# Optimization experiments

Measured on AMD Instinct MI355X. Metric: run time of the kernel, lower is better.

## Reference

```python
import jax, jax.numpy as jnp
import numpy as np

# ---- forest structure (static) ----
B = 32                      # number of trees in the batch
DEPTH = 12                  # topological levels per tree
LEVELS = [2 ** d for d in range(DEPTH)]           # nodes per level (root=level 0)
STARTS = np.concatenate([[0], np.cumsum(LEVELS)[:-1]]).astype(int)
NPG = int(sum(LEVELS))      # 4095 nodes per graph, node 0 = root
N = B * NPG                 # 131040 total nodes
VOCAB = 20000               # dataset.PAD_TOKEN_VALUE + 1
PAD = VOCAB - 1             # padding_idx
E = 256                     # embedding_dim (x_size)
H = 256                     # lstm_output_dim (h_size)
C = 104                     # num_classes (extra_non_linear=None)


def setup_inputs() -> dict:
    key = jax.random.key(0)
    ks = jax.random.split(key, 8)
    # random parent in the previous level for every non-root node (irregular fan-in)
    rng = np.random.RandomState(0)
    par = np.full(N, -1, dtype=np.int64)
    for g in range(B):
        off = g * NPG
        for d in range(1, DEPTH):
            nd = LEVELS[d]
            par[off + STARTS[d]: off + STARTS[d] + nd] = (
                off + STARTS[d - 1] + rng.randint(0, LEVELS[d - 1], size=nd))
    s = 0.05
    return {
        'x': jax.random.randint(ks[0], (N,), 0, VOCAB),
        'par': jnp.asarray(par),
        'emb': jax.random.normal(ks[1], (VOCAB, E), jnp.float32) * s,
        'W_iou': jax.random.normal(ks[2], (3 * H, E), jnp.float32) * s,
        'U_iou': jax.random.normal(ks[3], (3 * H, H), jnp.float32) * s,
        'b_iou': jnp.zeros((1, 3 * H), jnp.float32),
        'U_f_w': jax.random.normal(ks[4], (H, H), jnp.float32) * s,
        'U_f_b': jnp.zeros((H,), jnp.float32),
        'lin_w': jax.random.normal(ks[5], (C, H), jnp.float32) * s,
        'lin_b': jnp.zeros((C,), jnp.float32),
    }


def _forward(x, par, emb, W_iou, U_iou, b_iou, U_f_w, U_f_b, lin_w, lin_b):
    emb = emb.at[PAD].set(0.0)                 # padding_idx row is zero
    x_vec = emb[x]                             # [N, E]
    iou = x_vec @ W_iou.T                      # [N, 3H], W_iou has no bias
    h = jnp.zeros((N, H), x_vec.dtype)
    c = jnp.zeros((N, H), x_vec.dtype)
    offs = jnp.arange(B) * NPG
    # topological propagation: leaves (deepest level) -> root, per generation
    for d in range(DEPTH - 1, -1, -1):
        nd = LEVELS[d]
        nids = (offs[:, None] + STARTS[d] + jnp.arange(nd)).reshape(-1)  # [B*nd]
        iou_n = iou[nids]
        if d < DEPTH - 1:
            nc = LEVELS[d + 1]
            cids = (offs[:, None] + STARTS[d + 1] + jnp.arange(nc)).reshape(-1)
            h_ch = h[cids]                     # mailbox gather of child states
            c_ch = c[cids]
            p = par[cids]                      # global parent id per child
            seg = (p // NPG) * nd + (p % NPG - STARTS[d])  # parent slot in this level
            f = jax.nn.sigmoid(h_ch @ U_f_w.T + U_f_b)     # per-child forget gate
            h_tild = jax.ops.segment_sum(h_ch, seg, num_segments=B * nd)
            c_agg = jax.ops.segment_sum(f * c_ch, seg, num_segments=B * nd)
            iou_n = iou_n + h_tild @ U_iou.T
            c_n = c_agg
        else:
            c_n = jnp.zeros((B * nd, H), x_vec.dtype)
        iou_n = iou_n + b_iou
        i, o, u = jnp.split(iou_n, 3, axis=1)
        c_new = jax.nn.sigmoid(i) * jnp.tanh(u) + c_n
        h_new = jax.nn.sigmoid(o) * jnp.tanh(c_new)
        h = h.at[nids].set(h_new)
        c = c.at[nids].set(c_new)
    roots = h[offs]                            # graph.ndata['h'][0] per graph
    return roots @ lin_w.T + lin_b             # [B, num_classes]


def reference(x, par, emb, W_iou, U_iou, b_iou, U_f_w, U_f_b, lin_w, lin_b):
    return _forward(x, par, emb, W_iou, U_iou, b_iou, U_f_w, U_f_b, lin_w, lin_b)
```

## Files before the change

kernel.cpp:

```cpp
#include <hip/hip_runtime.h>
#include <hip/hip_bf16.h>


#define B_G     32
#define NPG     4095
#define NTOT    (B_G * NPG)
#define NCLS    104
#define VOCAB   20000
#define PAD_TOK 19999
#define KCAP    24
#define LB(d)   (32 * ((1 << (d)) - 1))

typedef unsigned short u16;
typedef unsigned int   u32;
typedef __attribute__((ext_vector_type(8))) short bfrag8;
typedef __attribute__((ext_vector_type(4))) float ffrag4;

__device__ __forceinline__ float bf2f(u16 v) {
    union { u32 u; float f; } x; x.u = ((u32)v) << 16; return x.f;
}
__device__ __forceinline__ u16 f2bf(float f) {
    union { __hip_bfloat16 h; u16 u; } c; c.h = __float2bfloat16(f); return c.u;
}
__device__ __forceinline__ float loadv(const void* b, int i, int isf32) {
    return isf32 ? ((const float*)b)[i] : bf2f(((const u16*)b)[i]);
}
__device__ __forceinline__ float sigf(float x) { return 1.f / (1.f + __expf(-x)); }

__global__ void probe_kernel(const void* emb, const void* Wiou, const void* Uiou,
                             const void* Ufw, const void* lw,
                             const int* x32, const int* par32, int* flags)
{
    if (threadIdx.x != 0 || blockIdx.x != 0) return;
    const void* ptrs[5] = { emb, Wiou, Uiou, Ufw, lw };
    for (int i = 0; i < 5; ++i) {
        const u16* p = (const u16*)ptrs[i];
        int big = 0;
        for (int k = 0; k < 128; ++k) {
            u32 e = (((u32)p[k]) << 16 >> 23) & 0xFF;
            if (e >= 129) ++big;
        }
        flags[i] = (big >= 4) ? 1 : 0;
    }
    int zx = 1;
    for (int k = 1; k <= 15; k += 2) if (x32[k] != 0) zx = 0;
    flags[5] = zx;
    flags[6] = (par32[3] == 0 && par32[5] == 0) ? 1 : 0;
}

__global__ __launch_bounds__(256) void prep_kernel(
    const int* __restrict__ x, const int* __restrict__ par,
    int* __restrict__ tokLvl, int* __restrict__ cnt, int* __restrict__ bucket,
    const int* __restrict__ flags)
{
    int gid = blockIdx.x * 256 + threadIdx.x;
    if (gid >= NTOT) return;
    int g     = (int)((u32)gid / NPG);
    int local = gid - g * NPG;
    int v  = local + 1;
    int d  = 31 - __clz(v);
    int j  = local - ((1 << d) - 1);
    int tok = flags[5] ? x[2 * gid] : x[gid];
    if (tok < 0 || tok >= VOCAB) tok = PAD_TOK;
    tokLvl[LB(d) + (g << d) + j] = tok;
    if (local > 0) {
        int p  = flags[6] ? par[2 * gid] : par[gid];
        p = max(0, min(p, NTOT - 1));
        int pg = (int)((u32)p / NPG);
        int pl = p - pg * NPG;
        int pd = d - 1;
        int ps = LB(pd) + (pg << pd) + (pl - ((1 << pd) - 1));
        ps = max(0, min(ps, 65503));
        int slot = atomicAdd(&cnt[ps], 1);
        if (slot < KCAP) bucket[(size_t)ps * KCAP + slot] = (g << d) + j;
    }
}

__global__ __launch_bounds__(256) void embconv_kernel(
    const void* __restrict__ emb, u16* __restrict__ embb,
    const int* __restrict__ flags)
{
    int i8 = (blockIdx.x * 256 + threadIdx.x) * 8;
    if (i8 >= VOCAB * 256) return;
    u16 v[8];
    if ((i8 >> 8) == PAD_TOK) {
        #pragma unroll
        for (int s = 0; s < 8; ++s) v[s] = 0;
    } else if (flags[0]) {
        const float* e = (const float*)emb + i8;
        float4 a = *(const float4*)e;
        float4 b = *(const float4*)(e + 4);
        v[0]=f2bf(a.x); v[1]=f2bf(a.y); v[2]=f2bf(a.z); v[3]=f2bf(a.w);
        v[4]=f2bf(b.x); v[5]=f2bf(b.y); v[6]=f2bf(b.z); v[7]=f2bf(b.w);
    } else {
        *(uint4*)v = *(const uint4*)((const u16*)emb + i8);
    }
    *(uint4*)(embb + i8) = *(uint4*)v;
}

__global__ __launch_bounds__(256) void wuc_kernel(
    const void* __restrict__ Wiou, const void* __restrict__ Uiou,
    u16* __restrict__ wuc, const int* __restrict__ flags)
{
    int idx = blockIdx.x * 256 + threadIdx.x;
    if (idx >= 16 * 768 * 32) return;
    int c   = idx / 24576;
    int rem = idx - c * 24576;
    int out = rem >> 5;
    int kk  = rem & 31;
    int k   = c * 32 + kk;
    float v = (k < 256) ? loadv(Wiou, out * 256 + k, flags[1])
                        : loadv(Uiou, out * 256 + (k - 256), flags[2]);
    wuc[idx] = f2bf(v);
}

__global__ __launch_bounds__(256) void ufc_kernel(
    const void* __restrict__ Ufw, u16* __restrict__ ufc,
    const int* __restrict__ flags)
{
    int idx = blockIdx.x * 256 + threadIdx.x;
    if (idx >= 8 * 256 * 32) return;
    int c   = idx >> 13;
    int rem = idx & 8191;
    int out = rem >> 5;
    int kk  = rem & 31;
    ufc[idx] = f2bf(loadv(Ufw, out * 256 + c * 32 + kk, flags[3]));
}

__global__ __launch_bounds__(256, 3) void gemm1_kernel(
    const u16* __restrict__ hch, u16* cbuf,
    const u16* __restrict__ ufc, const void* __restrict__ ufb,
    const int* __restrict__ flags)
{
    __shared__ u16 As[64][40];
    __shared__ u16 Bs[256][40];
    const int t = threadIdx.x;
    const int w = t >> 6, lane = t & 63, quad = lane >> 4, l15 = lane & 15;
    const int m0 = blockIdx.x * 64;
    const int f_uf = flags[3];

    ffrag4 acc[4][4];
    #pragma unroll
    for (int i = 0; i < 4; ++i)
        #pragma unroll
        for (int j = 0; j < 4; ++j) acc[i][j] = (ffrag4)0.f;

    const int arow = t >> 2, aseg = t & 3;
    for (int c = 0; c < 8; ++c) {
        *(uint4*)&As[arow][aseg * 8] =
            *(const uint4*)(hch + (size_t)(m0 + arow) * 256 + c * 32 + aseg * 8);
        #pragma unroll
        for (int r16 = 0; r16 < 4; ++r16) {
            int row = r16 * 64 + arow;
            *(uint4*)&Bs[row][aseg * 8] =
                *(const uint4*)(ufc + ((size_t)c * 256 + row) * 32 + aseg * 8);
        }
        __syncthreads();
        bfrag8 a[4], b[4];
        #pragma unroll
        for (int mt = 0; mt < 4; ++mt) a[mt] = *(bfrag8*)&As[mt * 16 + l15][quad * 8];
        #pragma unroll
        for (int nt = 0; nt < 4; ++nt) b[nt] = *(bfrag8*)&Bs[w * 64 + nt * 16 + l15][quad * 8];
        #pragma unroll
        for (int mt = 0; mt < 4; ++mt)
            #pragma unroll
            for (int nt = 0; nt < 4; ++nt)
                acc[mt][nt] = __builtin_amdgcn_mfma_f32_16x16x32_bf16(a[mt], b[nt], acc[mt][nt], 0, 0, 0);
        __syncthreads();
    }

    #pragma unroll
    for (int nt = 0; nt < 4; ++nt) {
        int hu = w * 64 + nt * 16 + l15;
        float fb = loadv(ufb, hu, f_uf);
        #pragma unroll
        for (int mt = 0; mt < 4; ++mt) {
            #pragma unroll
            for (int r = 0; r < 4; ++r) {
                int node = m0 + mt * 16 + quad * 4 + r;
                size_t off = (size_t)node * 256 + hu;
                float f = sigf(acc[mt][nt][r] + fb);
                cbuf[off] = f2bf(f * bf2f(cbuf[off]));
            }
        }
    }
}

__global__ __launch_bounds__(256) void agg_kernel(
    int NN, const u32* __restrict__ hch32, const u32* __restrict__ fcch32,
    const int* __restrict__ cnt_d, const int* __restrict__ bucket_d,
    u32* __restrict__ htild32, u32* __restrict__ cagg32)
{
    int pi  = blockIdx.x * 2 + (threadIdx.x >> 7);
    int col = threadIdx.x & 127;
    if (pi >= NN) return;
    int nc = min(cnt_d[pi], KCAP);
    float h0 = 0.f, h1 = 0.f, c0 = 0.f, c1 = 0.f;
    for (int ci = 0; ci < nc; ++ci) {
        int ch = bucket_d[(size_t)pi * KCAP + ci];
        u32 hv = hch32[(size_t)ch * 128 + col];
        u32 fv = fcch32[(size_t)ch * 128 + col];
        h0 += bf2f((u16)(hv & 0xffff)); h1 += bf2f((u16)(hv >> 16));
        c0 += bf2f((u16)(fv & 0xffff)); c1 += bf2f((u16)(fv >> 16));
    }
    htild32[(size_t)pi * 128 + col] = (u32)f2bf(h0) | ((u32)f2bf(h1) << 16);
    cagg32[(size_t)pi * 128 + col]  = (u32)f2bf(c0) | ((u32)f2bf(c1) << 16);
}

__global__ __launch_bounds__(256, 3) void gemm2_kernel(
    int nchunk, int NN,
    const int* __restrict__ tokLvl_d, const u16* __restrict__ embb,
    const u16* __restrict__ wuc, const void* __restrict__ biou,
    const u16* __restrict__ htild, const u16* __restrict__ cagg,
    u16* __restrict__ hdst, u16* __restrict__ cdst,
    const int* __restrict__ flags)
{
    __shared__ u16 As[128][40];
    __shared__ u16 Bs[192][40];
    __shared__ int toks[128];
    const int t = threadIdx.x;
    const int w = t >> 6, lane = t & 63, quad = lane >> 4, l15 = lane & 15;
    const int m0 = blockIdx.x * 128;
    const int q  = blockIdx.y;
    const int f_b = flags[1];

    if (t < 128) toks[t] = tokLvl_d[m0 + t];
    __syncthreads();

    ffrag4 acc[8][3];
    #pragma unroll
    for (int i = 0; i < 8; ++i)
        #pragma unroll
        for (int j = 0; j < 3; ++j) acc[i][j] = (ffrag4)0.f;

    const int arow = t >> 1, ac0 = (t & 1) * 16;
    const int brow = t >> 2, bseg = t & 3;
    for (int c = 0; c < nchunk; ++c) {
        if (c < 8) {
            const u16* e = embb + (size_t)toks[arow] * 256 + c * 32 + ac0;
            *(uint4*)&As[arow][ac0]     = *(const uint4*)e;
            *(uint4*)&As[arow][ac0 + 8] = *(const uint4*)(e + 8);
        } else {
            const u16* hsrc = htild + (size_t)(m0 + arow) * 256 + (c - 8) * 32 + ac0;
            *(uint4*)&As[arow][ac0]     = *(const uint4*)hsrc;
            *(uint4*)&As[arow][ac0 + 8] = *(const uint4*)(hsrc + 8);
        }
        #pragma unroll
        for (int g = 0; g < 3; ++g) {
            *(uint4*)&Bs[g * 64 + brow][bseg * 8] =
                *(const uint4*)(wuc + ((size_t)c * 768 + g * 256 + q * 64 + brow) * 32 + bseg * 8);
        }
        __syncthreads();
        bfrag8 a[8], b[3];
        #pragma unroll
        for (int mt = 0; mt < 8; ++mt) a[mt] = *(bfrag8*)&As[mt * 16 + l15][quad * 8];
        #pragma unroll
        for (int g = 0; g < 3; ++g) b[g] = *(bfrag8*)&Bs[g * 64 + w * 16 + l15][quad * 8];
        #pragma unroll
        for (int mt = 0; mt < 8; ++mt)
            #pragma unroll
            for (int g = 0; g < 3; ++g)
                acc[mt][g] = __builtin_amdgcn_mfma_f32_16x16x32_bf16(a[mt], b[g], acc[mt][g], 0, 0, 0);
        __syncthreads();
    }

    const int hu = q * 64 + w * 16 + l15;
    const float bi = loadv(biou, hu,       f_b);
    const float bo = loadv(biou, 256 + hu, f_b);
    const float bu = loadv(biou, 512 + hu, f_b);
    #pragma unroll
    for (int mt = 0; mt < 8; ++mt) {
        #pragma unroll
        for (int r = 0; r < 4; ++r) {
            int node = m0 + mt * 16 + quad * 4 + r;
            if (node < NN) {
                size_t off = (size_t)node * 256 + hu;
                float iv = acc[mt][0][r] + bi;
                float ov = acc[mt][1][r] + bo;
                float uv = acc[mt][2][r] + bu;
                float cg = cagg ? bf2f(cagg[off]) : 0.f;
                float cn = sigf(iv) * tanhf(uv) + cg;
                float hn = sigf(ov) * tanhf(cn);
                hdst[off] = f2bf(hn);
                cdst[off] = f2bf(cn);
            }
        }
    }
}

__global__ __launch_bounds__(1024, 1) void tail_kernel(
    const int* __restrict__ tokLvl, const u16* __restrict__ embb,
    const u16* __restrict__ wuc, const void* __restrict__ biou,
    const u16* __restrict__ ufc, const void* __restrict__ ufb,
    const u16* __restrict__ hB, const u16* __restrict__ cB,
    const int* __restrict__ cnt, const int* __restrict__ bucket,
    const void* __restrict__ lw, const void* __restrict__ lb,
    float* __restrict__ out, const int* __restrict__ flags)
{
    __shared__ u16 hs[64][264];
    __shared__ u16 cs[64][264];
    __shared__ u16 hts[32][264];
    __shared__ u16 cts[32][264];
    const int t = threadIdx.x;
    const int g = blockIdx.x;
    const int w = t >> 6;
    const int lane = t & 63, quad = lane >> 4, l15 = lane & 15;
    const int f_uf = flags[3], f_b = flags[1], f_lw = flags[4];

    #pragma unroll 1
    for (int i = t; i < 64 * 32; i += 1024) {
        int j = i >> 5, seg = i & 31;
        size_t off = (((size_t)((g << 6) + j)) << 8) + seg * 8;
        *(uint4*)&hs[j][seg * 8] = *(const uint4*)(hB + off);
        *(uint4*)&cs[j][seg * 8] = *(const uint4*)(cB + off);
    }
    __syncthreads();

    #pragma unroll 1
    for (int d = 5; d >= 0; --d) {
        const int ncr = 1 << (d + 1);
        const int np  = 1 << d;
        const int lvb = LB(d) + (g << d);
        const int hu  = w * 16 + l15;

        {
            ffrag4 facc[4];
            #pragma unroll
            for (int i = 0; i < 4; ++i) facc[i] = (ffrag4)0.f;
            #pragma unroll 2
            for (int c = 0; c < 8; ++c) {
                bfrag8 a[4];
                #pragma unroll
                for (int mt = 0; mt < 4; ++mt)
                    a[mt] = *(const bfrag8*)&hs[mt * 16 + l15][c * 32 + quad * 8];
                bfrag8 b = *(const bfrag8*)(ufc + ((size_t)c * 256 + w * 16 + l15) * 32 + quad * 8);
                #pragma unroll
                for (int mt = 0; mt < 4; ++mt)
                    facc[mt] = __builtin_amdgcn_mfma_f32_16x16x32_bf16(a[mt], b, facc[mt], 0, 0, 0);
            }
            float fb = loadv(ufb, hu, f_uf);
            #pragma unroll
            for (int mt = 0; mt < 4; ++mt) {
                #pragma unroll
                for (int r = 0; r < 4; ++r) {
                    int j = mt * 16 + quad * 4 + r;
                    if (j < ncr) {
                        float f = sigf(facc[mt][r] + fb);
                        cs[j][hu] = f2bf(f * bf2f(cs[j][hu]));
                    }
                }
            }
        }
        __syncthreads();

        {
            const int col = t & 127;
            #pragma unroll 1
            for (int pi = t >> 7; pi < np; pi += 8) {
                int nc = min(cnt[lvb + pi], KCAP);
                const int* bk = bucket + (size_t)(lvb + pi) * KCAP;
                float h0 = 0.f, h1 = 0.f, c0 = 0.f, c1 = 0.f;
                #pragma unroll 1
                for (int ci = 0; ci < nc; ++ci) {
                    int j = bk[ci] & (ncr - 1);
                    u32 hv = *(const u32*)&hs[j][col * 2];
                    u32 cv = *(const u32*)&cs[j][col * 2];
                    h0 += bf2f((u16)(hv & 0xffff)); h1 += bf2f((u16)(hv >> 16));
                    c0 += bf2f((u16)(cv & 0xffff)); c1 += bf2f((u16)(cv >> 16));
                }
                *(u32*)&hts[pi][col * 2] = (u32)f2bf(h0) | ((u32)f2bf(h1) << 16);
                *(u32*)&cts[pi][col * 2] = (u32)f2bf(c0) | ((u32)f2bf(c1) << 16);
            }
        }
        __syncthreads();

        {
            int tok0 = tokLvl[lvb + min(l15, np - 1)];
            int tok1 = tokLvl[lvb + min(16 + l15, np - 1)];
            ffrag4 acc[2][3];
            #pragma unroll
            for (int i = 0; i < 2; ++i)
                #pragma unroll
                for (int j = 0; j < 3; ++j) acc[i][j] = (ffrag4)0.f;
            #pragma unroll 2
            for (int c = 0; c < 16; ++c) {
                bfrag8 a0, a1;
                if (c < 8) {
                    a0 = *(const bfrag8*)(embb + (size_t)tok0 * 256 + c * 32 + quad * 8);
                    a1 = *(const bfrag8*)(embb + (size_t)tok1 * 256 + c * 32 + quad * 8);
                } else {
                    a0 = *(const bfrag8*)&hts[l15][(c - 8) * 32 + quad * 8];
                    a1 = *(const bfrag8*)&hts[16 + l15][(c - 8) * 32 + quad * 8];
                }
                #pragma unroll
                for (int g3 = 0; g3 < 3; ++g3) {
                    bfrag8 b = *(const bfrag8*)(wuc + ((size_t)c * 768 + g3 * 256 + w * 16 + l15) * 32 + quad * 8);
                    acc[0][g3] = __builtin_amdgcn_mfma_f32_16x16x32_bf16(a0, b, acc[0][g3], 0, 0, 0);
                    acc[1][g3] = __builtin_amdgcn_mfma_f32_16x16x32_bf16(a1, b, acc[1][g3], 0, 0, 0);
                }
            }
            float bi = loadv(biou, hu,       f_b);
            float bo = loadv(biou, 256 + hu, f_b);
            float bu = loadv(biou, 512 + hu, f_b);
            #pragma unroll
            for (int mt = 0; mt < 2; ++mt) {
                #pragma unroll
                for (int r = 0; r < 4; ++r) {
                    int p = mt * 16 + quad * 4 + r;
                    if (p < np) {
                        float iv = acc[mt][0][r] + bi;
                        float ov = acc[mt][1][r] + bo;
                        float uv = acc[mt][2][r] + bu;
                        float cn = sigf(iv) * tanhf(uv) + bf2f(cts[p][hu]);
                        float hn = sigf(ov) * tanhf(cn);
                        hs[p][hu] = f2bf(hn);
                        cs[p][hu] = f2bf(cn);
                    }
                }
            }
        }
        __syncthreads();
    }

    if (t < NCLS) {
        float acc = 0.f;
        #pragma unroll 1
        for (int k = 0; k < 256; ++k)
            acc += loadv(lw, t * 256 + k, f_lw) * bf2f(hs[0][k]);
        out[(size_t)g * NCLS + t] = acc + loadv(lb, t, f_lw);
    }
}

__global__ void fill_kernel(float* out, int n, float v) {
    int i = blockIdx.x * 256 + threadIdx.x;
    if (i < n) out[i] = v;
}

extern "C" void kernel_launch(void* const* d_in, const int* in_sizes, int n_in,
                              void* d_out, int out_size, void* d_ws, size_t ws_size,
                              hipStream_t stream)
{
    float* out = (float*)d_out;

    static const int exp_sizes[10] = {131040, 131040, 5120000, 196608, 196608,
                                      768, 65536, 256, 26624, 104};
    bool shapes_ok = (n_in == 10) && (out_size == B_G * NCLS);
    for (int i = 0; i < 10 && shapes_ok; ++i)
        if (in_sizes[i] != exp_sizes[i]) shapes_ok = false;
    if (!shapes_ok) {
        fill_kernel<<<(out_size + 255) / 256, 256, 0, stream>>>(out, out_size, 2.0f);
        return;
    }

    const int* x     = (const int*)d_in[0];
    const int* par   = (const int*)d_in[1];
    const void* emb  = d_in[2];
    const void* Wiou = d_in[3];
    const void* Uiou = d_in[4];
    const void* biou = d_in[5];
    const void* Ufw  = d_in[6];
    const void* Ufb  = d_in[7];
    const void* lw   = d_in[8];
    const void* lb   = d_in[9];

    char* W = (char*)d_ws;
    u16* hA     = (u16*)(W + 0);
    u16* hB     = (u16*)(W + 33554432);
    u16* cA     = (u16*)(W + 50331648);
    u16* cB     = (u16*)(W + 83886080);
    u16* htild  = (u16*)(W + 100663296);
    u16* cagg   = (u16*)(W + 117440512);
    u16* WUc    = (u16*)(W + 134217728);
    u16* Ufc    = (u16*)(W + 135004160);
    int* tokLvl = (int*)(W + 135135232);
    int* cnt    = (int*)(W + 135659520);
    int* bucket = (int*)(W + 135921664);
    u16* embb   = (u16*)(W + 142213120);
    int* flags  = (int*)(W + 152453120);
    const size_t NEED = 152453184;
    if (ws_size < NEED) {
        fill_kernel<<<(out_size + 255) / 256, 256, 0, stream>>>(out, out_size, 1.0f);
        return;
    }

    hipMemsetAsync(cnt, 0, 65536 * sizeof(int), stream);
    probe_kernel<<<1, 1, 0, stream>>>(emb, Wiou, Uiou, Ufw, lw, x, par, flags);
    prep_kernel<<<(NTOT + 255) / 256, 256, 0, stream>>>(x, par, tokLvl, cnt, bucket, flags);
    embconv_kernel<<<2500, 256, 0, stream>>>(emb, embb, flags);
    wuc_kernel<<<1536, 256, 0, stream>>>(Wiou, Uiou, WUc, flags);
    ufc_kernel<<<256, 256, 0, stream>>>(Ufw, Ufc, flags);

    gemm2_kernel<<<dim3(512, 4), 256, 0, stream>>>(
        8, 65536, tokLvl + LB(11), embb, WUc, biou,
        nullptr, nullptr, hA, cA, flags);

    for (int d = 10; d >= 6; --d) {
        const int cl = d + 1;
        const int NC = B_G << cl;
        const int NN = B_G << d;
        const u16* hch = (cl & 1) ? hA : hB;
        u16*       cch = (cl & 1) ? cA : cB;
        u16* hdst = (d & 1) ? hA : hB;
        u16* cdst = (d & 1) ? cA : cB;
        gemm1_kernel<<<NC / 64, 256, 0, stream>>>(hch, cch, Ufc, Ufb, flags);
        agg_kernel<<<(NN + 1) / 2, 256, 0, stream>>>(
            NN, (const u32*)hch, (const u32*)cch,
            cnt + LB(d), bucket + (size_t)LB(d) * KCAP,
            (u32*)htild, (u32*)cagg);
        gemm2_kernel<<<dim3((NN + 127) / 128, 4), 256, 0, stream>>>(
            16, NN, tokLvl + LB(d), embb, WUc, biou,
            htild, cagg, hdst, cdst, flags);
    }

    tail_kernel<<<B_G, 1024, 0, stream>>>(
        tokLvl, embb, WUc, biou, Ufc, Ufb,
        hB, cB, cnt, bucket, lw, lb, out, flags);
}
```

Baseline: 704.9 us.

## Merge prep kernels, parallelize probe, drop fused tail kernel for per-level launches

Merges the embedding, weight-layout and tree-prep kernels into one multi-role launch and rewrites the format probe to use one wavefront per tensor with ballots. The single-block-per-tree tail kernel that handled levels 5..0 in shared memory is removed. Those levels now run through the generic gemm1/agg/gemm2 launches, and a small linear kernel computes the classifier. This cuts launch count at the front but adds about 18 small launches for the shallow levels, each with very little work.

```diff
diff --git a/kernel.cpp b/kernel.cpp
--- a/kernel.cpp
+++ b/kernel.cpp
@@ -11,6 +11,12 @@
 #define KCAP    24
 #define LB(d)   (32 * ((1 << (d)) - 1))
 
+#define EMB_BLKS  2500
+#define WUC_BLKS  1536
+#define UFC_BLKS  256
+#define PREP_BLKS 512
+#define CONV_BLKS (EMB_BLKS + WUC_BLKS + UFC_BLKS + PREP_BLKS)
+
 typedef unsigned short u16;
 typedef unsigned int   u32;
 typedef __attribute__((ext_vector_type(8))) short bfrag8;
@@ -27,104 +33,105 @@
 }
 __device__ __forceinline__ float sigf(float x) { return 1.f / (1.f + __expf(-x)); }
 
-__global__ void probe_kernel(const void* emb, const void* Wiou, const void* Uiou,
-                             const void* Ufw, const void* lw,
-                             const int* x32, const int* par32, int* flags)
-{
-    if (threadIdx.x != 0 || blockIdx.x != 0) return;
+__global__ __launch_bounds__(384) void probe_kernel(
+    const void* emb, const void* Wiou, const void* Uiou,
+    const void* Ufw, const void* lw,
+    const int* x32, const int* par32, int* flags)
+{
+    if (blockIdx.x != 0) return;
+    const int w = threadIdx.x >> 6, lane = threadIdx.x & 63;
     const void* ptrs[5] = { emb, Wiou, Uiou, Ufw, lw };
-    for (int i = 0; i < 5; ++i) {
-        const u16* p = (const u16*)ptrs[i];
+    if (w < 5) {
+        const u16* p = (const u16*)ptrs[w];
         int big = 0;
-        for (int k = 0; k < 128; ++k) {
-            u32 e = (((u32)p[k]) << 16 >> 23) & 0xFF;
+        #pragma unroll
+        for (int k = 0; k < 2; ++k) {
+            u32 e = (((u32)p[lane * 2 + k]) << 16 >> 23) & 0xFF;
             if (e >= 129) ++big;
         }
-        flags[i] = (big >= 4) ? 1 : 0;
-    }
-    int zx = 1;
-    for (int k = 1; k <= 15; k += 2) if (x32[k] != 0) zx = 0;
-    flags[5] = zx;
-    flags[6] = (par32[3] == 0 && par32[5] == 0) ? 1 : 0;
-}
-
-__global__ __launch_bounds__(256) void prep_kernel(
+        unsigned long long m1 = __ballot(big >= 1);
+        unsigned long long m2 = __ballot(big >= 2);
+        int tot = __popcll(m1) + __popcll(m2);
+        if (lane == 0) flags[w] = (tot >= 4) ? 1 : 0;
+    } else if (w == 5) {
+        int bad = (lane < 8) ? (x32[2 * lane + 1] != 0) : 0;
+        unsigned long long mx = __ballot(bad != 0);
+        if (lane == 0) {
+            flags[5] = (mx == 0) ? 1 : 0;
+            flags[6] = (par32[3] == 0 && par32[5] == 0) ? 1 : 0;
+        }
+    }
+}
+
+__global__ __launch_bounds__(256) void convert_kernel(
+    const void* __restrict__ emb, u16* __restrict__ embb,
+    const void* __restrict__ Wiou, const void* __restrict__ Uiou,
+    u16* __restrict__ wuc,
+    const void* __restrict__ Ufw, u16* __restrict__ ufc,
     const int* __restrict__ x, const int* __restrict__ par,
     int* __restrict__ tokLvl, int* __restrict__ cnt, int* __restrict__ bucket,
     const int* __restrict__ flags)
 {
-    int gid = blockIdx.x * 256 + threadIdx.x;
-    if (gid >= NTOT) return;
-    int g     = (int)((u32)gid / NPG);
-    int local = gid - g * NPG;
-    int v  = local + 1;
-    int d  = 31 - __clz(v);
-    int j  = local - ((1 << d) - 1);
-    int tok = flags[5] ? x[2 * gid] : x[gid];
-    if (tok < 0 || tok >= VOCAB) tok = PAD_TOK;
-    tokLvl[LB(d) + (g << d) + j] = tok;
-    if (local > 0) {
-        int p  = flags[6] ? par[2 * gid] : par[gid];
-        p = max(0, min(p, NTOT - 1));
-        int pg = (int)((u32)p / NPG);
-        int pl = p - pg * NPG;
-        int pd = d - 1;
-        int ps = LB(pd) + (pg << pd) + (pl - ((1 << pd) - 1));
-        ps = max(0, min(ps, 65503));
-        int slot = atomicAdd(&cnt[ps], 1);
-        if (slot < KCAP) bucket[(size_t)ps * KCAP + slot] = (g << d) + j;
-    }
-}
-
-__global__ __launch_bounds__(256) void embconv_kernel(
-    const void* __restrict__ emb, u16* __restrict__ embb,
-    const int* __restrict__ flags)
-{
-    int i8 = (blockIdx.x * 256 + threadIdx.x) * 8;
-    if (i8 >= VOCAB * 256) return;
-    u16 v[8];
-    if ((i8 >> 8) == PAD_TOK) {
-        #pragma unroll
-        for (int s = 0; s < 8; ++s) v[s] = 0;
-    } else if (flags[0]) {
-        const float* e = (const float*)emb + i8;
-        float4 a = *(const float4*)e;
-        float4 b = *(const float4*)(e + 4);
-        v[0]=f2bf(a.x); v[1]=f2bf(a.y); v[2]=f2bf(a.z); v[3]=f2bf(a.w);
-        v[4]=f2bf(b.x); v[5]=f2bf(b.y); v[6]=f2bf(b.z); v[7]=f2bf(b.w);
+    const int b = blockIdx.x;
+    if (b < EMB_BLKS) {
+        int i8 = (b * 256 + (int)threadIdx.x) * 8;
+        if (i8 >= VOCAB * 256) return;
+        u16 v[8];
+        if ((i8 >> 8) == PAD_TOK) {
+            #pragma unroll
+            for (int s = 0; s < 8; ++s) v[s] = 0;
+        } else if (flags[0]) {
+            const float* e = (const float*)emb + i8;
+            float4 a = *(const float4*)e;
+            float4 c = *(const float4*)(e + 4);
+            v[0]=f2bf(a.x); v[1]=f2bf(a.y); v[2]=f2bf(a.z); v[3]=f2bf(a.w);
+            v[4]=f2bf(c.x); v[5]=f2bf(c.y); v[6]=f2bf(c.z); v[7]=f2bf(c.w);
+        } else {
+            *(uint4*)v = *(const uint4*)((const u16*)emb + i8);
+        }
+        *(uint4*)(embb + i8) = *(uint4*)v;
+    } else if (b < EMB_BLKS + WUC_BLKS) {
+        int idx = (b - EMB_BLKS) * 256 + (int)threadIdx.x;
+        if (idx >= 16 * 768 * 32) return;
+        int c   = idx / 24576;
+        int rem = idx - c * 24576;
+        int out = rem >> 5;
+        int kk  = rem & 31;
+        int k   = c * 32 + kk;
+        float v = (k < 256) ? loadv(Wiou, out * 256 + k, flags[1])
+                            : loadv(Uiou, out * 256 + (k - 256), flags[2]);
+        wuc[idx] = f2bf(v);
+    } else if (b < EMB_BLKS + WUC_BLKS + UFC_BLKS) {
+        int idx = (b - EMB_BLKS - WUC_BLKS) * 256 + (int)threadIdx.x;
+        if (idx >= 8 * 256 * 32) return;
+        int c   = idx >> 13;
+        int rem = idx & 8191;
+        int out = rem >> 5;
+        int kk  = rem & 31;
+        ufc[idx] = f2bf(loadv(Ufw, out * 256 + c * 32 + kk, flags[3]));
     } else {
-        *(uint4*)v = *(const uint4*)((const u16*)emb + i8);
-    }
-    *(uint4*)(embb + i8) = *(uint4*)v;
-}
-
-__global__ __launch_bounds__(256) void wuc_kernel(
-    const void* __restrict__ Wiou, const void* __restrict__ Uiou,
-    u16* __restrict__ wuc, const int* __restrict__ flags)
-{
-    int idx = blockIdx.x * 256 + threadIdx.x;
-    if (idx >= 16 * 768 * 32) return;
-    int c   = idx / 24576;
-    int rem = idx - c * 24576;
-    int out = rem >> 5;
-    int kk  = rem & 31;
-    int k   = c * 32 + kk;
-    float v = (k < 256) ? loadv(Wiou, out * 256 + k, flags[1])
-                        : loadv(Uiou, out * 256 + (k - 256), flags[2]);
-    wuc[idx] = f2bf(v);
-}
-
-__global__ __launch_bounds__(256) void ufc_kernel(
-    const void* __restrict__ Ufw, u16* __restrict__ ufc,
-    const int* __restrict__ flags)
-{
-    int idx = blockIdx.x * 256 + threadIdx.x;
-    if (idx >= 8 * 256 * 32) return;
-    int c   = idx >> 13;
-    int rem = idx & 8191;
-    int out = rem >> 5;
-    int kk  = rem & 31;
-    ufc[idx] = f2bf(loadv(Ufw, out * 256 + c * 32 + kk, flags[3]));
+        int gid = (b - EMB_BLKS - WUC_BLKS - UFC_BLKS) * 256 + (int)threadIdx.x;
+        if (gid >= NTOT) return;
+        int g     = (int)((u32)gid / NPG);
+        int local = gid - g * NPG;
+        int v  = local + 1;
+        int d  = 31 - __clz(v);
+        int j  = local - ((1 << d) - 1);
+        int tok = flags[5] ? x[2 * gid] : x[gid];
+        if (tok < 0 || tok >= VOCAB) tok = PAD_TOK;
+        tokLvl[LB(d) + (g << d) + j] = tok;
+        if (local > 0) {
+            int p  = flags[6] ? par[2 * gid] : par[gid];
+            p = max(0, min(p, NTOT - 1));
+            int pg = (int)((u32)p / NPG);
+            int pl = p - pg * NPG;
+            int pd = d - 1;
+            int ps = LB(pd) + (pg << pd) + (pl - ((1 << pd) - 1));
+            ps = max(0, min(ps, 65503));
+            int slot = atomicAdd(&cnt[ps], 1);
+            if (slot < KCAP) bucket[(size_t)ps * KCAP + slot] = (g << d) + j;
+        }
+    }
 }
 
 __global__ __launch_bounds__(256, 3) void gemm1_kernel(
@@ -288,145 +295,25 @@
     }
 }
 
-__global__ __launch_bounds__(1024, 1) void tail_kernel(
-    const int* __restrict__ tokLvl, const u16* __restrict__ embb,
-    const u16* __restrict__ wuc, const void* __restrict__ biou,
-    const u16* __restrict__ ufc, const void* __restrict__ ufb,
-    const u16* __restrict__ hB, const u16* __restrict__ cB,
-    const int* __restrict__ cnt, const int* __restrict__ bucket,
-    const void* __restrict__ lw, const void* __restrict__ lb,
-    float* __restrict__ out, const int* __restrict__ flags)
-{
-    __shared__ u16 hs[64][264];
-    __shared__ u16 cs[64][264];
-    __shared__ u16 hts[32][264];
-    __shared__ u16 cts[32][264];
-    const int t = threadIdx.x;
-    const int g = blockIdx.x;
-    const int w = t >> 6;
-    const int lane = t & 63, quad = lane >> 4, l15 = lane & 15;
-    const int f_uf = flags[3], f_b = flags[1], f_lw = flags[4];
-
-    #pragma unroll 1
-    for (int i = t; i < 64 * 32; i += 1024) {
-        int j = i >> 5, seg = i & 31;
-        size_t off = (((size_t)((g << 6) + j)) << 8) + seg * 8;
-        *(uint4*)&hs[j][seg * 8] = *(const uint4*)(hB + off);
-        *(uint4*)&cs[j][seg * 8] = *(const uint4*)(cB + off);
+__global__ __launch_bounds__(128) void linear_kernel(
+    const u16* __restrict__ hroot, const void* __restrict__ lw,
+    const void* __restrict__ lb, float* __restrict__ out,
+    const int* __restrict__ flags)
+{
+    __shared__ float hrow[256];
+    const int g = blockIdx.x, t = threadIdx.x;
+    const int f_lw = flags[4];
+    {
+        u32 v = *(const u32*)(hroot + (size_t)g * 256 + t * 2);
+        hrow[t * 2]     = bf2f((u16)(v & 0xffff));
+        hrow[t * 2 + 1] = bf2f((u16)(v >> 16));
     }
     __syncthreads();
-
-    #pragma unroll 1
-    for (int d = 5; d >= 0; --d) {
-        const int ncr = 1 << (d + 1);
-        const int np  = 1 << d;
-        const int lvb = LB(d) + (g << d);
-        const int hu  = w * 16 + l15;
-
-        {
-            ffrag4 facc[4];
-            #pragma unroll
-            for (int i = 0; i < 4; ++i) facc[i] = (ffrag4)0.f;
-            #pragma unroll 2
-            for (int c = 0; c < 8; ++c) {
-                bfrag8 a[4];
-                #pragma unroll
-                for (int mt = 0; mt < 4; ++mt)
-                    a[mt] = *(const bfrag8*)&hs[mt * 16 + l15][c * 32 + quad * 8];
-                bfrag8 b = *(const bfrag8*)(ufc + ((size_t)c * 256 + w * 16 + l15) * 32 + quad * 8);
-                #pragma unroll
-                for (int mt = 0; mt < 4; ++mt)
-                    facc[mt] = __builtin_amdgcn_mfma_f32_16x16x32_bf16(a[mt], b, facc[mt], 0, 0, 0);
-            }
-            float fb = loadv(ufb, hu, f_uf);
-            #pragma unroll
-            for (int mt = 0; mt < 4; ++mt) {
-                #pragma unroll
-                for (int r = 0; r < 4; ++r) {
-                    int j = mt * 16 + quad * 4 + r;
-                    if (j < ncr) {
-                        float f = sigf(facc[mt][r] + fb);
-                        cs[j][hu] = f2bf(f * bf2f(cs[j][hu]));
-                    }
-                }
-            }
-        }
-        __syncthreads();
-
-        {
-            const int col = t & 127;
-            #pragma unroll 1
-            for (int pi = t >> 7; pi < np; pi += 8) {
-                int nc = min(cnt[lvb + pi], KCAP);
-                const int* bk = bucket + (size_t)(lvb + pi) * KCAP;
-                float h0 = 0.f, h1 = 0.f, c0 = 0.f, c1 = 0.f;
-                #pragma unroll 1
-                for (int ci = 0; ci < nc; ++ci) {
-                    int j = bk[ci] & (ncr - 1);
-                    u32 hv = *(const u32*)&hs[j][col * 2];
-                    u32 cv = *(const u32*)&cs[j][col * 2];
-                    h0 += bf2f((u16)(hv & 0xffff)); h1 += bf2f((u16)(hv >> 16));
-                    c0 += bf2f((u16)(cv & 0xffff)); c1 += bf2f((u16)(cv >> 16));
-                }
-                *(u32*)&hts[pi][col * 2] = (u32)f2bf(h0) | ((u32)f2bf(h1) << 16);
-                *(u32*)&cts[pi][col * 2] = (u32)f2bf(c0) | ((u32)f2bf(c1) << 16);
-            }
-        }
-        __syncthreads();
-
-        {
-            int tok0 = tokLvl[lvb + min(l15, np - 1)];
-            int tok1 = tokLvl[lvb + min(16 + l15, np - 1)];
-            ffrag4 acc[2][3];
-            #pragma unroll
-            for (int i = 0; i < 2; ++i)
-                #pragma unroll
-                for (int j = 0; j < 3; ++j) acc[i][j] = (ffrag4)0.f;
-            #pragma unroll 2
-            for (int c = 0; c < 16; ++c) {
-                bfrag8 a0, a1;
-                if (c < 8) {
-                    a0 = *(const bfrag8*)(embb + (size_t)tok0 * 256 + c * 32 + quad * 8);
-                    a1 = *(const bfrag8*)(embb + (size_t)tok1 * 256 + c * 32 + quad * 8);
-                } else {
-                    a0 = *(const bfrag8*)&hts[l15][(c - 8) * 32 + quad * 8];
-                    a1 = *(const bfrag8*)&hts[16 + l15][(c - 8) * 32 + quad * 8];
-                }
-                #pragma unroll
-                for (int g3 = 0; g3 < 3; ++g3) {
-                    bfrag8 b = *(const bfrag8*)(wuc + ((size_t)c * 768 + g3 * 256 + w * 16 + l15) * 32 + quad * 8);
-                    acc[0][g3] = __builtin_amdgcn_mfma_f32_16x16x32_bf16(a0, b, acc[0][g3], 0, 0, 0);
-                    acc[1][g3] = __builtin_amdgcn_mfma_f32_16x16x32_bf16(a1, b, acc[1][g3], 0, 0, 0);
-                }
-            }
-            float bi = loadv(biou, hu,       f_b);
-            float bo = loadv(biou, 256 + hu, f_b);
-            float bu = loadv(biou, 512 + hu, f_b);
-            #pragma unroll
-            for (int mt = 0; mt < 2; ++mt) {
-                #pragma unroll
-                for (int r = 0; r < 4; ++r) {
-                    int p = mt * 16 + quad * 4 + r;
-                    if (p < np) {
-                        float iv = acc[mt][0][r] + bi;
-                        float ov = acc[mt][1][r] + bo;
-                        float uv = acc[mt][2][r] + bu;
-                        float cn = sigf(iv) * tanhf(uv) + bf2f(cts[p][hu]);
-                        float hn = sigf(ov) * tanhf(cn);
-                        hs[p][hu] = f2bf(hn);
-                        cs[p][hu] = f2bf(cn);
-                    }
-                }
-            }
-        }
-        __syncthreads();
-    }
-
     if (t < NCLS) {
         float acc = 0.f;
-        #pragma unroll 1
+        #pragma unroll 4
         for (int k = 0; k < 256; ++k)
-            acc += loadv(lw, t * 256 + k, f_lw) * bf2f(hs[0][k]);
+            acc += loadv(lw, t * 256 + k, f_lw) * hrow[k];
         out[(size_t)g * NCLS + t] = acc + loadv(lb, t, f_lw);
     }
 }
@@ -484,17 +371,16 @@
     }
 
     hipMemsetAsync(cnt, 0, 65536 * sizeof(int), stream);
-    probe_kernel<<<1, 1, 0, stream>>>(emb, Wiou, Uiou, Ufw, lw, x, par, flags);
-    prep_kernel<<<(NTOT + 255) / 256, 256, 0, stream>>>(x, par, tokLvl, cnt, bucket, flags);
-    embconv_kernel<<<2500, 256, 0, stream>>>(emb, embb, flags);
-    wuc_kernel<<<1536, 256, 0, stream>>>(Wiou, Uiou, WUc, flags);
-    ufc_kernel<<<256, 256, 0, stream>>>(Ufw, Ufc, flags);
+    probe_kernel<<<1, 384, 0, stream>>>(emb, Wiou, Uiou, Ufw, lw, x, par, flags);
+    convert_kernel<<<CONV_BLKS, 256, 0, stream>>>(
+        emb, embb, Wiou, Uiou, WUc, Ufw, Ufc,
+        x, par, tokLvl, cnt, bucket, flags);
 
     gemm2_kernel<<<dim3(512, 4), 256, 0, stream>>>(
         8, 65536, tokLvl + LB(11), embb, WUc, biou,
         nullptr, nullptr, hA, cA, flags);
 
-    for (int d = 10; d >= 6; --d) {
+    for (int d = 10; d >= 0; --d) {
         const int cl = d + 1;
         const int NC = B_G << cl;
         const int NN = B_G << d;
@@ -512,7 +398,5 @@
             htild, cagg, hdst, cdst, flags);
     }
 
-    tail_kernel<<<B_G, 1024, 0, stream>>>(
-        tokLvl, embb, WUc, biou, Ufc, Ufb,
-        hB, cB, cnt, bucket, lw, lb, out, flags);
-}
+    linear_kernel<<<B_G, 128, 0, stream>>>(hB, lw, lb, out, flags);
+}
```

After: 828.3 us. 1.18x slower.
